# Performance work log

Measured on AMD Instinct MI355X. Metric: run time of the kernel, lower is better.

Reference implementation:

```python
import jax, jax.numpy as jnp
import numpy as np

S, T, SP = 4096, 64, 48          # spatial, temporal, seqPredict
P = T - SP                        # predictLength = 16
INP, EMB_H, EMB = 3, 64, 128      # input size, embedding hidden, embedding size
HID, OUT = 256, 128               # LSTM hidden, outputLayer size
FC1, FC2, LG = 256, 64, 32        # output FCNet dims, laneGate hidden


def setup_inputs() -> dict:
    key = jax.random.key(0)
    ks = jax.random.split(key, 32)
    def w(k, shape, fan_in):
        return jax.random.normal(k, shape, dtype=jnp.float32) / np.sqrt(fan_in)
    inp = {}
    inp["inputData"] = jax.random.normal(ks[0], (S, T, INP), dtype=jnp.float32)
    inp["lane"] = jax.random.uniform(ks[1], (S, 1), dtype=jnp.float32)
    # laneGate FCNet: 1 -> LG -> 1
    inp["lgW1"] = w(ks[2], (LG, 1), 1); inp["lgb1"] = jnp.zeros((LG,), jnp.float32)
    inp["lgW2"] = w(ks[3], (1, LG), LG); inp["lgb2"] = jnp.zeros((1,), jnp.float32)
    # embedding FCNet: INP -> EMB_H -> EMB
    inp["eW1"] = w(ks[4], (EMB_H, INP), INP); inp["eb1"] = jnp.zeros((EMB_H,), jnp.float32)
    inp["eW2"] = w(ks[5], (EMB, EMB_H), EMB_H); inp["eb2"] = jnp.zeros((EMB,), jnp.float32)
    # LSTMCell (gate order i, f, g, o)
    inp["Wih"] = w(ks[6], (4 * HID, EMB), EMB)
    inp["Whh"] = w(ks[7], (4 * HID, HID), HID)
    inp["bih"] = jnp.zeros((4 * HID,), jnp.float32)
    inp["bhh"] = jnp.zeros((4 * HID,), jnp.float32)
    # Conv1d(1,1,3,padding=1)
    inp["convw"] = w(ks[8], (3,), 3)
    inp["convb"] = jnp.zeros((1,), jnp.float32)
    # outputLayer: HID -> OUT
    inp["oW"] = w(ks[9], (OUT, HID), HID); inp["ob"] = jnp.zeros((OUT,), jnp.float32)
    # outputs FCNet (addLayer): OUT -> FC1 -> FC2 -> 1
    inp["fW1"] = w(ks[10], (FC1, OUT), OUT); inp["fb1"] = jnp.zeros((FC1,), jnp.float32)
    inp["fW2"] = w(ks[11], (FC2, FC1), FC1); inp["fb2"] = jnp.zeros((FC2,), jnp.float32)
    inp["fW3"] = w(ks[12], (1, FC2), FC2); inp["fb3"] = jnp.zeros((1,), jnp.float32)
    return inp


def reference(inputData, lane, lgW1, lgb1, lgW2, lgb2, eW1, eb1, eW2, eb2,
              Wih, Whh, bih, bhh, convw, convb, oW, ob,
              fW1, fb1, fW2, fb2, fW3, fb3):
    # laneGate: FCNet(1->LG->1) then sigmoid
    lg = jax.nn.relu(lane @ lgW1.T + lgb1) @ lgW2.T + lgb2
    laneC = jax.nn.sigmoid(lg)                       # [S, 1]
    x = inputData * laneC[:, :, None]                # [S, T, INP]
    # embedding FCNet + outer relu
    emb = jax.nn.relu(jax.nn.relu(x @ eW1.T + eb1) @ eW2.T + eb2)  # [S, T, EMB]
    xs = jnp.transpose(emb, (1, 0, 2))               # [T, S, EMB]

    def convpool(h):
        hp = jnp.pad(h, ((0, 0), (1, 1)))
        return convw[0] * hp[:, :-2] + convw[1] * hp[:, 1:-1] + convw[2] * hp[:, 2:] + convb[0]

    def step(carry, x_t):
        h, c = carry
        g = x_t @ Wih.T + bih + h @ Whh.T + bhh      # [S, 4*HID]
        i, f, gg, o = jnp.split(g, 4, axis=-1)
        c = jax.nn.sigmoid(f) * c + jax.nn.sigmoid(i) * jnp.tanh(gg)
        h = jax.nn.sigmoid(o) * jnp.tanh(c)
        h = convpool(h)
        return (h, c), (h, c)

    h0 = jnp.zeros((S, HID), jnp.float32)
    c0 = jnp.zeros((S, HID), jnp.float32)
    # loop 1: time 0 .. SP inclusive (SP+1 steps)
    (h1, c1), (Hs1, Cs1) = jax.lax.scan(step, (h0, c0), xs[:SP + 1])
    # loop 2: time SP .. T-1 (re-processes step SP, overwriting H[:,:,SP])
    (_, _), (Hs2, Cs2) = jax.lax.scan(step, (h1, c1), xs[SP:])

    H = jnp.transpose(jnp.concatenate([Hs1[:SP], Hs2], axis=0), (1, 2, 0))  # [S, HID, T]
    C = jnp.transpose(jnp.concatenate([Cs1[:SP], Cs2], axis=0), (1, 2, 0))

    predict_h = jnp.transpose(Hs2, (1, 0, 2)).reshape(S * P, HID)
    out = predict_h @ oW.T + ob                      # [S*P, OUT]
    out = jax.nn.relu(out @ fW1.T + fb1)
    out = jax.nn.relu(out @ fW2.T + fb2)
    out = out @ fW3.T + fb3                          # [S*P, 1]
    output = out.reshape(S, P) / laneC               # [S, P]
    return (output, H, C)
```

## Files before the change

### kernel.cpp

```cpp
#include <hip/hip_runtime.h>
#include <hip/hip_bf16.h>
#include <stdint.h>

using f32x4  = __attribute__((ext_vector_type(4))) float;
using bf16x8 = __attribute__((ext_vector_type(8))) __bf16;
using short8 = __attribute__((ext_vector_type(8))) short;

__device__ __forceinline__ short f2b(float f) {
    unsigned u = __builtin_bit_cast(unsigned, f);
    unsigned r = (u + 0x7fff + ((u >> 16) & 1)) >> 16;
    return (short)r;
}
__device__ __forceinline__ float b2f(short s) {
    unsigned u = ((unsigned)(unsigned short)s) << 16;
    return __builtin_bit_cast(float, u);
}
__device__ __forceinline__ float sigf(float x) {
    return __builtin_amdgcn_rcpf(1.f + __expf(-x));
}
__device__ __forceinline__ float tanhf_fast(float x) {
    x = fminf(fmaxf(x, -15.f), 15.f);
    return 2.f * __builtin_amdgcn_rcpf(1.f + __expf(-2.f * x)) - 1.f;
}

__global__ __launch_bounds__(256) void lanec_k(const float* lane, const float* W1, const float* b1,
                                               const float* W2, const float* b2, float* laneC) {
    int s = blockIdx.x * 256 + threadIdx.x;
    float v = lane[s];
    float acc = b2[0];
    #pragma unroll
    for (int k = 0; k < 32; ++k) {
        float t = fmaxf(v * W1[k] + b1[k], 0.f);
        acc += t * W2[k];
    }
    laneC[s] = 1.f / (1.f + __expf(-acc));
}

__global__ __launch_bounds__(256) void pack_k(const float* Wih, const float* Whh, const float* bih,
                                              const float* bhh, const float* oW, const float* fW1,
                                              const float* fW2, const float* eW2,
                                              short* pW2, float* biasP,
                                              short* oWp, short* fW1p, short* fW2p, short* eW2p) {
    int i = blockIdx.x * 256 + threadIdx.x;
    if (i < 393216) {
        int e = i & 7, l = (i >> 3) & 63, fg = (i >> 9) & 63, kc = i >> 15;
        int w = fg >> 3, f = fg & 7;
        int lj = l & 15, lk = l >> 4;
        int g = f >> 1, u = f & 1;
        int j = 32 * w + 16 * u + lj;
        int n = g * 256 + j;
        int k = kc * 32 + lk * 8 + e;
        pW2[i] = f2b(k < 128 ? Wih[n * 128 + k] : Whh[n * 256 + (k - 128)]);
        return;
    }
    i -= 393216;
    if (i < 1024) {
        int lj = i & 15, f = (i >> 4) & 7, w = i >> 7;
        int g = f >> 1, u = f & 1;
        int j = 32 * w + 16 * u + lj;
        int n = g * 256 + j;
        biasP[i] = bih[n] + bhh[n];
        return;
    }
    i -= 1024;
    if (i < 32768) { oWp[i] = f2b(oW[i]); return; }
    i -= 32768;
    if (i < 32768) { fW1p[i] = f2b(fW1[i]); return; }
    i -= 32768;
    if (i < 32768) {
        int n = i / 256;
        fW2p[i] = (n < 64) ? f2b(fW2[i]) : (short)0;
        return;
    }
    i -= 32768;
    if (i < 8192) { eW2p[i] = f2b(eW2[i]); return; }
}

__global__ __launch_bounds__(256) void embed1_k(const float* inp, const float* laneC,
                                                const float* eW1, const float* eb1, short* h1) {
    int g = threadIdx.x >> 6, j = threadIdx.x & 63;
    int t = blockIdx.x >> 10;
    int s = ((blockIdx.x & 1023) << 2) + g;
    float lc = laneC[s];
    size_t rin = ((size_t)s * 64 + t) * 3;
    float x0 = inp[rin] * lc, x1 = inp[rin + 1] * lc, x2 = inp[rin + 2] * lc;
    float h = fmaxf(eW1[j * 3] * x0 + eW1[j * 3 + 1] * x1 + eW1[j * 3 + 2] * x2 + eb1[j], 0.f);
    h1[((size_t)t * 4096 + s) * 64 + j] = f2b(h);
}

__global__ __launch_bounds__(256) void gemm_k(const short* A1, int K1, const short* A2, int K2,
                                              const short* B, int Kt, const float* bias,
                                              float* outF, short* outB, int Nstore, int Nreal,
                                              int relu) {
    __shared__ alignas(16) short As[128 * 32];
    __shared__ alignas(16) short Bs[128 * 32];
    int tid = threadIdx.x;
    int wave = tid >> 6, lane = tid & 63;
    int m0 = blockIdx.x * 128, n0 = blockIdx.y * 128;

    f32x4 acc[4][4];
    #pragma unroll
    for (int i = 0; i < 4; ++i)
        #pragma unroll
        for (int j = 0; j < 4; ++j) acc[i][j] = (f32x4){0.f, 0.f, 0.f, 0.f};

    const int lr = lane & 15, lk8 = (lane >> 4) * 8;
    const int am = (wave & 1) * 64, bn = (wave >> 1) * 64;
    const int row = tid >> 2, c8 = (tid & 3) * 8;
    int nK = Kt / 32;

    for (int kt = 0; kt < nK; ++kt) {
        int kk = kt * 32;
        const short* Asrc; int astr, acol;
        if (kk < K1) { Asrc = A1; astr = K1; acol = kk; }
        else         { Asrc = A2; astr = K2; acol = kk - K1; }
        short8 a0 = *(const short8*)(Asrc + (size_t)(m0 + row) * astr + acol + c8);
        short8 a1 = *(const short8*)(Asrc + (size_t)(m0 + 64 + row) * astr + acol + c8);
        short8 b0 = *(const short8*)(B + (size_t)(n0 + row) * Kt + kk + c8);
        short8 b1 = *(const short8*)(B + (size_t)(n0 + 64 + row) * Kt + kk + c8);
        __syncthreads();
        *(short8*)&As[tid * 8] = a0;
        *(short8*)&As[(tid + 256) * 8] = a1;
        *(short8*)&Bs[tid * 8] = b0;
        *(short8*)&Bs[(tid + 256) * 8] = b1;
        __syncthreads();
        bf16x8 af[4], bfr[4];
        #pragma unroll
        for (int i = 0; i < 4; ++i) af[i]  = *(const bf16x8*)&As[(am + i * 16 + lr) * 32 + lk8];
        #pragma unroll
        for (int j = 0; j < 4; ++j) bfr[j] = *(const bf16x8*)&Bs[(bn + j * 16 + lr) * 32 + lk8];
        #pragma unroll
        for (int i = 0; i < 4; ++i)
            #pragma unroll
            for (int j = 0; j < 4; ++j)
                acc[i][j] = __builtin_amdgcn_mfma_f32_16x16x32_bf16(af[i], bfr[j], acc[i][j], 0, 0, 0);
    }

    int r0 = m0 + am + (lane >> 4) * 4;
    int c0 = n0 + bn + (lane & 15);
    #pragma unroll
    for (int j = 0; j < 4; ++j) {
        int col = c0 + j * 16;
        if (col >= Nreal) continue;
        float bs = bias[col];
        #pragma unroll
        for (int i = 0; i < 4; ++i) {
            #pragma unroll
            for (int r = 0; r < 4; ++r) {
                int rw = r0 + i * 16 + r;
                float v = acc[i][j][r] + bs;
                if (relu) v = fmaxf(v, 0.f);
                size_t o = (size_t)rw * Nstore + col;
                if (outF) outF[o] = v;
                if (outB) outB[o] = f2b(v);
            }
        }
    }
}

__global__ __launch_bounds__(512, 2) void lstm_k(const short* xs, const short* pW2, const float* biasP,
                                                 const float* convw, const float* convb,
                                                 float* Hd, float* Cd, short* predictb, int staged) {
    __shared__ alignas(16) short Wbuf[2][32768];
    __shared__ alignas(16) short h_lds[4096];
    __shared__ float hraw[16][258];

    const int tid = threadIdx.x;
    const int w = tid >> 6, l = tid & 63;
    const int lj = l & 15, lk = l >> 4;
    const int s0 = blockIdx.x * 16;

    bf16x8 wreg[4][8];
    #pragma unroll
    for (int kc = 0; kc < 4; ++kc)
        #pragma unroll
        for (int f = 0; f < 8; ++f)
            wreg[kc][f] = *(const bf16x8*)(pW2 + (size_t)((kc * 64 + w * 8 + f) * 64 + l) * 8);
    float biasv[8];
    #pragma unroll
    for (int f = 0; f < 8; ++f) biasv[f] = biasP[w * 128 + f * 16 + lj];
    float creg[2][4] = {{0.f, 0.f, 0.f, 0.f}, {0.f, 0.f, 0.f, 0.f}};
    const float cw0 = convw[0], cw1 = convw[1], cw2 = convw[2], cb = convb[0];

    for (int i = tid; i < 4096; i += 512) h_lds[i] = 0;
    if (tid < 16) { hraw[tid][0] = 0.f; hraw[tid][257] = 0.f; }
    __syncthreads();

    short* WbufF = &Wbuf[0][0];
    auto issue_chunk = [&](int c, int pp) {
        const short* src = pW2 + (size_t)c * 32768 + tid * 8;
        short* dst = WbufF + pp * 32768 + tid * 8;
        #pragma unroll
        for (int ri = 0; ri < 8; ++ri)
            __builtin_amdgcn_global_load_lds(
                (const __attribute__((address_space(1))) void*)(src + ri * 4096),
                (__attribute__((address_space(3))) void*)(dst + ri * 4096), 16, 0, 0);
    };

    int p = 0;
    issue_chunk(4, 0);

    for (int k = 0; k < 65; ++k) {
        int it = (k <= 48) ? k : k - 1;
        const short* xrow = xs + ((size_t)it * 4096 + s0 + lj) * 128 + lk * 8;
        bf16x8 ax0 = *(const bf16x8*)(xrow);
        bf16x8 ax1 = *(const bf16x8*)(xrow + 32);
        bf16x8 ax2 = *(const bf16x8*)(xrow + 64);
        bf16x8 ax3 = *(const bf16x8*)(xrow + 96);

        f32x4 acc[8];
        #pragma unroll
        for (int f = 0; f < 8; ++f) acc[f] = (f32x4){biasv[f], biasv[f], biasv[f], biasv[f]};
        #pragma unroll
        for (int f = 0; f < 8; ++f) acc[f] = __builtin_amdgcn_mfma_f32_16x16x32_bf16(ax0, wreg[0][f], acc[f], 0, 0, 0);
        #pragma unroll
        for (int f = 0; f < 8; ++f) acc[f] = __builtin_amdgcn_mfma_f32_16x16x32_bf16(ax1, wreg[1][f], acc[f], 0, 0, 0);
        #pragma unroll
        for (int f = 0; f < 8; ++f) acc[f] = __builtin_amdgcn_mfma_f32_16x16x32_bf16(ax2, wreg[2][f], acc[f], 0, 0, 0);
        #pragma unroll
        for (int f = 0; f < 8; ++f) acc[f] = __builtin_amdgcn_mfma_f32_16x16x32_bf16(ax3, wreg[3][f], acc[f], 0, 0, 0);

        #pragma unroll
        for (int cc = 0; cc < 8; ++cc) {
            asm volatile("s_waitcnt vmcnt(0)" ::: "memory");
            __syncthreads();
            issue_chunk(cc < 7 ? cc + 5 : 4, p ^ 1);
            bf16x8 ah = *(const bf16x8*)&h_lds[((cc * 4 + lk) * 16 + lj) * 8];
            #pragma unroll
            for (int f = 0; f < 8; ++f) {
                bf16x8 wf = *(const bf16x8*)(WbufF + p * 32768 + ((w * 8 + f) * 64 + l) * 8);
                acc[f] = __builtin_amdgcn_mfma_f32_16x16x32_bf16(ah, wf, acc[f], 0, 0, 0);
            }
            p ^= 1;
        }

        int tslot = (k < 48) ? k : k - 1;
        int doW = (k != 48);
        int pslot = k - 49;
        #pragma unroll
        for (int u = 0; u < 2; ++u) {
            int j = 32 * w + 16 * u + lj;
            #pragma unroll
            for (int r = 0; r < 4; ++r) {
                int s = 4 * lk + r;
                float gi = acc[0 + u][r], gf = acc[2 + u][r];
                float gg = acc[4 + u][r], go = acc[6 + u][r];
                float c = sigf(gf) * creg[u][r] + sigf(gi) * tanhf_fast(gg);
                creg[u][r] = c;
                hraw[s][j + 1] = sigf(go) * tanhf_fast(c);
                if (doW) {
                    size_t o = staged ? ((((size_t)(s0 + s) * 64 + tslot) << 8) + j)
                                      : ((((size_t)(s0 + s) << 8) + j) * 64 + tslot);
                    Cd[o] = c;
                }
            }
        }
        __syncthreads();

        #pragma unroll
        for (int u = 0; u < 2; ++u) {
            int j = 32 * w + 16 * u + lj;
            int elbase = ((w * 4 + 2 * u + (lj >> 3)) * 16) * 8 + (lj & 7);
            #pragma unroll
            for (int r = 0; r < 4; ++r) {
                int s = 4 * lk + r;
                float h = cw0 * hraw[s][j] + cw1 * hraw[s][j + 1] + cw2 * hraw[s][j + 2] + cb;
                h_lds[elbase + s * 8] = f2b(h);
                if (doW) {
                    size_t o = staged ? ((((size_t)(s0 + s) * 64 + tslot) << 8) + j)
                                      : ((((size_t)(s0 + s) << 8) + j) * 64 + tslot);
                    Hd[o] = h;
                }
                if (pslot >= 0) predictb[(((size_t)(s0 + s) * 16 + pslot) << 8) + j] = f2b(h);
            }
        }
        __syncthreads();
    }
}

__global__ __launch_bounds__(256) void transpose_k(const float* Hs, const float* Cs,
                                                   float* Ho, float* Co) {
    __shared__ float tile[64][129];
    int s = blockIdx.x, jh = blockIdx.y;
    const float* src = blockIdx.z ? Cs : Hs;
    float* dst = blockIdx.z ? Co : Ho;
    #pragma unroll 4
    for (int i = 0; i < 32; ++i) {
        int idx = i * 256 + threadIdx.x;
        int t = idx >> 7, jj = idx & 127;
        tile[t][jj] = src[((size_t)s * 64 + t) * 256 + jh * 128 + jj];
    }
    __syncthreads();
    #pragma unroll 4
    for (int i = 0; i < 32; ++i) {
        int idx = i * 256 + threadIdx.x;
        int jj = idx >> 6, t = idx & 63;
        dst[((size_t)s * 256 + jh * 128 + jj) * 64 + t] = tile[t][jj];
    }
}

__global__ __launch_bounds__(256) void final_k(const short* t2b, const float* fW3, const float* fb3,
                                               const float* laneC, float* out0) {
    int r = blockIdx.x * 256 + threadIdx.x;
    float acc = fb3[0];
    const short* rowp = t2b + (size_t)r * 64;
    #pragma unroll 8
    for (int k = 0; k < 64; ++k) acc += b2f(rowp[k]) * fW3[k];
    out0[r] = acc / laneC[r >> 4];
}

extern "C" void kernel_launch(void* const* d_in, const int* in_sizes, int n_in,
                              void* d_out, int out_size, void* d_ws, size_t ws_size,
                              hipStream_t stream) {
    (void)in_sizes; (void)n_in; (void)out_size;
    const float* inputData = (const float*)d_in[0];
    const float* lane  = (const float*)d_in[1];
    const float* lgW1  = (const float*)d_in[2];  const float* lgb1 = (const float*)d_in[3];
    const float* lgW2  = (const float*)d_in[4];  const float* lgb2 = (const float*)d_in[5];
    const float* eW1   = (const float*)d_in[6];  const float* eb1  = (const float*)d_in[7];
    const float* eW2   = (const float*)d_in[8];  const float* eb2  = (const float*)d_in[9];
    const float* Wih   = (const float*)d_in[10]; const float* Whh  = (const float*)d_in[11];
    const float* bih   = (const float*)d_in[12]; const float* bhh  = (const float*)d_in[13];
    const float* convw = (const float*)d_in[14]; const float* convb= (const float*)d_in[15];
    const float* oW    = (const float*)d_in[16]; const float* ob   = (const float*)d_in[17];
    const float* fW1   = (const float*)d_in[18]; const float* fb1  = (const float*)d_in[19];
    const float* fW2   = (const float*)d_in[20]; const float* fb2  = (const float*)d_in[21];
    const float* fW3   = (const float*)d_in[22]; const float* fb3  = (const float*)d_in[23];

    float* out0 = (float*)d_out;
    float* Hout = out0 + 65536;
    float* Cout = Hout + (size_t)67108864;

    char* w = (char*)d_ws;
    size_t off = 0;
    auto alloc = [&](size_t bytes) -> void* {
        void* p = w + off;
        off += (bytes + 255) & ~(size_t)255;
        return p;
    };
    float* laneC    = (float*)alloc(4096 * 4);
    float* biasP    = (float*)alloc(1024 * 4);
    short* pW2      = (short*)alloc((size_t)1024 * 384 * 2);
    short* oWp      = (short*)alloc((size_t)128 * 256 * 2);
    short* fW1p     = (short*)alloc((size_t)256 * 128 * 2);
    short* fW2p     = (short*)alloc((size_t)128 * 256 * 2);
    short* eW2p     = (short*)alloc((size_t)128 * 64 * 2);
    short* h1       = (short*)alloc((size_t)64 * 4096 * 64 * 2);
    short* xs       = (short*)alloc((size_t)64 * 4096 * 128 * 2);
    short* predictb = (short*)alloc((size_t)65536 * 256 * 2);
    short* t0b      = (short*)alloc((size_t)65536 * 128 * 2);
    short* t1b      = (short*)alloc((size_t)65536 * 256 * 2);
    short* t2b      = (short*)alloc((size_t)65536 * 64 * 2);
    float* Hstage   = (float*)alloc((size_t)4096 * 64 * 256 * 4);
    float* Cstage   = (float*)alloc((size_t)4096 * 64 * 256 * 4);
    bool staged = ws_size >= off;

    lanec_k<<<16, 256, 0, stream>>>(lane, lgW1, lgb1, lgW2, lgb2, laneC);
    {
        int total = 393216 + 1024 + 32768 + 32768 + 32768 + 8192;
        pack_k<<<(total + 255) / 256, 256, 0, stream>>>(Wih, Whh, bih, bhh, oW, fW1, fW2, eW2,
                                                        pW2, biasP, oWp, fW1p, fW2p, eW2p);
    }
    embed1_k<<<65536, 256, 0, stream>>>(inputData, laneC, eW1, eb1, h1);
    gemm_k<<<dim3(2048, 1), 256, 0, stream>>>(h1, 64, (const short*)nullptr, 0, eW2p, 64,
                                              eb2, (float*)nullptr, xs, 128, 128, 1);

    float* Hd = staged ? Hstage : Hout;
    float* Cd = staged ? Cstage : Cout;
    lstm_k<<<256, 512, 0, stream>>>(xs, pW2, biasP, convw, convb, Hd, Cd, predictb,
                                    staged ? 1 : 0);
    if (staged)
        transpose_k<<<dim3(4096, 2, 2), 256, 0, stream>>>(Hstage, Cstage, Hout, Cout);

    gemm_k<<<dim3(512, 1), 256, 0, stream>>>(predictb, 256, (const short*)nullptr, 0, oWp, 256,
                                             ob, (float*)nullptr, t0b, 128, 128, 0);
    gemm_k<<<dim3(512, 2), 256, 0, stream>>>(t0b, 128, (const short*)nullptr, 0, fW1p, 128,
                                             fb1, (float*)nullptr, t1b, 256, 256, 1);
    gemm_k<<<dim3(512, 1), 256, 0, stream>>>(t1b, 256, (const short*)nullptr, 0, fW2p, 256,
                                             fb2, (float*)nullptr, t2b, 64, 64, 1);
    final_k<<<256, 256, 0, stream>>>(t2b, fW3, fb3, laneC, out0);
}
```

Before: 1.833 ms.

## Restructure LSTM kernel: 32 rows per block, streamed weights, shuffle conv, bf16 staging

The LSTM kernel now processes 32 spatial rows per block over 128 blocks instead of 16 rows over 256, so each streamed weight fragment feeds two MFMAs. The input-projection weights are no longer held in registers; all twelve K-chunks (input plus hidden) are double-buffered into LDS per wave. The depthwise conv across the hidden dimension uses lane shuffles plus small edge arrays instead of a full float LDS scratch. H and C are staged in bf16 before the transpose to float, which halves staging traffic but rounds the H/C outputs to bf16 precision. The unstaged fallback path is removed.

```diff
diff --git a/kernel.cpp b/kernel.cpp
--- a/kernel.cpp
+++ b/kernel.cpp
@@ -158,144 +158,176 @@
     }
 }
 
-__global__ __launch_bounds__(512, 2) void lstm_k(const short* xs, const short* pW2, const float* biasP,
+__global__ __launch_bounds__(512, 1) void lstm_k(const short* xs, const short* pW2, const float* biasP,
                                                  const float* convw, const float* convb,
-                                                 float* Hd, float* Cd, short* predictb, int staged) {
-    __shared__ alignas(16) short Wbuf[2][32768];
-    __shared__ alignas(16) short h_lds[4096];
-    __shared__ float hraw[16][258];
+                                                 short* Hd, short* Cd, short* predictb) {
+    __shared__ alignas(16) short Wbuf[2][8][4096];
+    __shared__ alignas(16) short hfrag[8192];
+    __shared__ float edgeA[8][32];
+    __shared__ float edgeB[8][32];
 
     const int tid = threadIdx.x;
     const int w = tid >> 6, l = tid & 63;
     const int lj = l & 15, lk = l >> 4;
-    const int s0 = blockIdx.x * 16;
-
-    bf16x8 wreg[4][8];
-    #pragma unroll
-    for (int kc = 0; kc < 4; ++kc)
-        #pragma unroll
-        for (int f = 0; f < 8; ++f)
-            wreg[kc][f] = *(const bf16x8*)(pW2 + (size_t)((kc * 64 + w * 8 + f) * 64 + l) * 8);
+    const int sb = blockIdx.x * 32;
+
     float biasv[8];
     #pragma unroll
     for (int f = 0; f < 8; ++f) biasv[f] = biasP[w * 128 + f * 16 + lj];
-    float creg[2][4] = {{0.f, 0.f, 0.f, 0.f}, {0.f, 0.f, 0.f, 0.f}};
+    float creg[2][2][4] = {};
     const float cw0 = convw[0], cw1 = convw[1], cw2 = convw[2], cb = convb[0];
 
-    for (int i = tid; i < 4096; i += 512) h_lds[i] = 0;
-    if (tid < 16) { hraw[tid][0] = 0.f; hraw[tid][257] = 0.f; }
+    for (int i = tid; i < 8192; i += 512) hfrag[i] = 0;
     __syncthreads();
 
-    short* WbufF = &Wbuf[0][0];
-    auto issue_chunk = [&](int c, int pp) {
-        const short* src = pW2 + (size_t)c * 32768 + tid * 8;
-        short* dst = WbufF + pp * 32768 + tid * 8;
+    auto issueW = [&](int kc, int pp) {
+        const short* src = pW2 + (((size_t)kc * 64 + w * 8) << 9) + l * 8;
+        short* dst = &Wbuf[pp][w][l * 8];
         #pragma unroll
         for (int ri = 0; ri < 8; ++ri)
             __builtin_amdgcn_global_load_lds(
-                (const __attribute__((address_space(1))) void*)(src + ri * 4096),
-                (__attribute__((address_space(3))) void*)(dst + ri * 4096), 16, 0, 0);
+                (const __attribute__((address_space(1))) void*)(src + ri * 512),
+                (__attribute__((address_space(3))) void*)(dst + ri * 512), 16, 0, 0);
     };
 
-    int p = 0;
-    issue_chunk(4, 0);
+    bf16x8 a[4][2];
+    auto loadA = [&](int it) {
+        #pragma unroll
+        for (int kc = 0; kc < 4; ++kc)
+            #pragma unroll
+            for (int rg = 0; rg < 2; ++rg)
+                a[kc][rg] = *(const bf16x8*)(xs + ((size_t)it * 4096 + sb + rg * 16 + lj) * 128
+                                             + kc * 32 + lk * 8);
+    };
+
+    loadA(0);
+    issueW(0, 0);
+    issueW(1, 1);
 
     for (int k = 0; k < 65; ++k) {
-        int it = (k <= 48) ? k : k - 1;
-        const short* xrow = xs + ((size_t)it * 4096 + s0 + lj) * 128 + lk * 8;
-        bf16x8 ax0 = *(const bf16x8*)(xrow);
-        bf16x8 ax1 = *(const bf16x8*)(xrow + 32);
-        bf16x8 ax2 = *(const bf16x8*)(xrow + 64);
-        bf16x8 ax3 = *(const bf16x8*)(xrow + 96);
-
-        f32x4 acc[8];
-        #pragma unroll
-        for (int f = 0; f < 8; ++f) acc[f] = (f32x4){biasv[f], biasv[f], biasv[f], biasv[f]};
-        #pragma unroll
-        for (int f = 0; f < 8; ++f) acc[f] = __builtin_amdgcn_mfma_f32_16x16x32_bf16(ax0, wreg[0][f], acc[f], 0, 0, 0);
-        #pragma unroll
-        for (int f = 0; f < 8; ++f) acc[f] = __builtin_amdgcn_mfma_f32_16x16x32_bf16(ax1, wreg[1][f], acc[f], 0, 0, 0);
-        #pragma unroll
-        for (int f = 0; f < 8; ++f) acc[f] = __builtin_amdgcn_mfma_f32_16x16x32_bf16(ax2, wreg[2][f], acc[f], 0, 0, 0);
-        #pragma unroll
-        for (int f = 0; f < 8; ++f) acc[f] = __builtin_amdgcn_mfma_f32_16x16x32_bf16(ax3, wreg[3][f], acc[f], 0, 0, 0);
-
-        #pragma unroll
-        for (int cc = 0; cc < 8; ++cc) {
-            asm volatile("s_waitcnt vmcnt(0)" ::: "memory");
-            __syncthreads();
-            issue_chunk(cc < 7 ? cc + 5 : 4, p ^ 1);
-            bf16x8 ah = *(const bf16x8*)&h_lds[((cc * 4 + lk) * 16 + lj) * 8];
+        const int itn = (k < 48) ? k + 1 : ((k < 64) ? k : 63);
+
+        f32x4 acc[2][8];
+        #pragma unroll
+        for (int rg = 0; rg < 2; ++rg)
+            #pragma unroll
+            for (int f = 0; f < 8; ++f)
+                acc[rg][f] = (f32x4){biasv[f], biasv[f], biasv[f], biasv[f]};
+
+        #pragma unroll
+        for (int kc = 0; kc < 12; ++kc) {
+            asm volatile("s_waitcnt vmcnt(8)" ::: "memory");
+            const int p = kc & 1;
+            bf16x8 af0, af1;
+            if (kc < 4) { af0 = a[kc][0]; af1 = a[kc][1]; }
+            else {
+                const int hc = kc - 4;
+                af0 = *(const bf16x8*)&hfrag[(((hc * 4 + lk) * 2 + 0) * 16 + lj) * 8];
+                af1 = *(const bf16x8*)&hfrag[(((hc * 4 + lk) * 2 + 1) * 16 + lj) * 8];
+            }
             #pragma unroll
             for (int f = 0; f < 8; ++f) {
-                bf16x8 wf = *(const bf16x8*)(WbufF + p * 32768 + ((w * 8 + f) * 64 + l) * 8);
-                acc[f] = __builtin_amdgcn_mfma_f32_16x16x32_bf16(ah, wf, acc[f], 0, 0, 0);
+                bf16x8 wf = *(const bf16x8*)&Wbuf[p][w][f * 512 + l * 8];
+                acc[0][f] = __builtin_amdgcn_mfma_f32_16x16x32_bf16(af0, wf, acc[0][f], 0, 0, 0);
+                acc[1][f] = __builtin_amdgcn_mfma_f32_16x16x32_bf16(af1, wf, acc[1][f], 0, 0, 0);
             }
-            p ^= 1;
+            if (kc == 9) loadA(itn);
+            if (kc <= 9) issueW(kc + 2, p);
+            else if (kc == 10) issueW(0, 0);
+            else issueW(1, 1);
         }
 
-        int tslot = (k < 48) ? k : k - 1;
-        int doW = (k != 48);
-        int pslot = k - 49;
-        #pragma unroll
-        for (int u = 0; u < 2; ++u) {
-            int j = 32 * w + 16 * u + lj;
+        float hr[2][2][4];
+        #pragma unroll
+        for (int rg = 0; rg < 2; ++rg)
+            #pragma unroll
+            for (int u = 0; u < 2; ++u)
+                #pragma unroll
+                for (int r = 0; r < 4; ++r) {
+                    float gi = acc[rg][u][r],     gf = acc[rg][2 + u][r];
+                    float gg = acc[rg][4 + u][r], go = acc[rg][6 + u][r];
+                    float c = sigf(gf) * creg[rg][u][r] + sigf(gi) * tanhf_fast(gg);
+                    creg[rg][u][r] = c;
+                    hr[rg][u][r] = sigf(go) * tanhf_fast(c);
+                }
+        if (lj == 0) {
+            #pragma unroll
+            for (int rg = 0; rg < 2; ++rg)
+                #pragma unroll
+                for (int r = 0; r < 4; ++r) edgeA[w][rg * 16 + 4 * lk + r] = hr[rg][0][r];
+        }
+        if (lj == 15) {
+            #pragma unroll
+            for (int rg = 0; rg < 2; ++rg)
+                #pragma unroll
+                for (int r = 0; r < 4; ++r) edgeB[w][rg * 16 + 4 * lk + r] = hr[rg][1][r];
+        }
+        asm volatile("s_waitcnt lgkmcnt(0)" ::: "memory");
+        __builtin_amdgcn_s_barrier();
+
+        const int tslot = (k < 48) ? k : k - 1;
+        const bool doW = (k != 48);
+        const int pslot = k - 49;
+        #pragma unroll
+        for (int rg = 0; rg < 2; ++rg)
             #pragma unroll
             for (int r = 0; r < 4; ++r) {
-                int s = 4 * lk + r;
-                float gi = acc[0 + u][r], gf = acc[2 + u][r];
-                float gg = acc[4 + u][r], go = acc[6 + u][r];
-                float c = sigf(gf) * creg[u][r] + sigf(gi) * tanhf_fast(gg);
-                creg[u][r] = c;
-                hraw[s][j + 1] = sigf(go) * tanhf_fast(c);
+                const int s = rg * 16 + 4 * lk + r;
+                float v0 = hr[rg][0][r], v1 = hr[rg][1][r];
+                float s0r = __shfl(v0, l + 1, 64);
+                float s0l = __shfl(v0, l - 1, 64);
+                float s1r = __shfl(v1, l + 1, 64);
+                float s1l = __shfl(v1, l - 1, 64);
+                float x01 = __shfl(v1, l - 15, 64);
+                float x10 = __shfl(v0, l + 15, 64);
+                float n0r = (lj < 15) ? s0r : x01;
+                float n0l = (lj > 0) ? s0l : (w > 0 ? edgeB[w - 1][s] : 0.f);
+                float n1r = (lj < 15) ? s1r : (w < 7 ? edgeA[w + 1][s] : 0.f);
+                float n1l = (lj > 0) ? s1l : x10;
+                float h0 = cw0 * n0l + cw1 * v0 + cw2 * n0r + cb;
+                float h1 = cw0 * n1l + cw1 * v1 + cw2 * n1r + cb;
+                const int j0 = 32 * w + lj, j1 = j0 + 16;
+                hfrag[(((w * 4 + 0 + (lj >> 3)) * 2 + rg) * 16 + 4 * lk + r) * 8 + (lj & 7)] = f2b(h0);
+                hfrag[(((w * 4 + 2 + (lj >> 3)) * 2 + rg) * 16 + 4 * lk + r) * 8 + (lj & 7)] = f2b(h1);
+                const int ss = sb + s;
                 if (doW) {
-                    size_t o = staged ? ((((size_t)(s0 + s) * 64 + tslot) << 8) + j)
-                                      : ((((size_t)(s0 + s) << 8) + j) * 64 + tslot);
-                    Cd[o] = c;
+                    size_t o0 = ((size_t)ss * 64 + tslot) * 256;
+                    Hd[o0 + j0] = f2b(h0);
+                    Hd[o0 + j1] = f2b(h1);
+                    Cd[o0 + j0] = f2b(creg[rg][0][r]);
+                    Cd[o0 + j1] = f2b(creg[rg][1][r]);
+                }
+                if (pslot >= 0) {
+                    size_t po = ((size_t)ss * 16 + pslot) * 256;
+                    predictb[po + j0] = f2b(h0);
+                    predictb[po + j1] = f2b(h1);
                 }
             }
-        }
-        __syncthreads();
-
-        #pragma unroll
-        for (int u = 0; u < 2; ++u) {
-            int j = 32 * w + 16 * u + lj;
-            int elbase = ((w * 4 + 2 * u + (lj >> 3)) * 16) * 8 + (lj & 7);
-            #pragma unroll
-            for (int r = 0; r < 4; ++r) {
-                int s = 4 * lk + r;
-                float h = cw0 * hraw[s][j] + cw1 * hraw[s][j + 1] + cw2 * hraw[s][j + 2] + cb;
-                h_lds[elbase + s * 8] = f2b(h);
-                if (doW) {
-                    size_t o = staged ? ((((size_t)(s0 + s) * 64 + tslot) << 8) + j)
-                                      : ((((size_t)(s0 + s) << 8) + j) * 64 + tslot);
-                    Hd[o] = h;
-                }
-                if (pslot >= 0) predictb[(((size_t)(s0 + s) * 16 + pslot) << 8) + j] = f2b(h);
-            }
-        }
-        __syncthreads();
-    }
-}
-
-__global__ __launch_bounds__(256) void transpose_k(const float* Hs, const float* Cs,
+        asm volatile("s_waitcnt lgkmcnt(0)" ::: "memory");
+        __builtin_amdgcn_s_barrier();
+    }
+    asm volatile("s_waitcnt vmcnt(0)" ::: "memory");
+}
+
+__global__ __launch_bounds__(256) void transpose_k(const short* Hs, const short* Cs,
                                                    float* Ho, float* Co) {
-    __shared__ float tile[64][129];
+    __shared__ short tile[64][132];
     int s = blockIdx.x, jh = blockIdx.y;
-    const float* src = blockIdx.z ? Cs : Hs;
+    const short* src = blockIdx.z ? Cs : Hs;
     float* dst = blockIdx.z ? Co : Ho;
     #pragma unroll 4
-    for (int i = 0; i < 32; ++i) {
+    for (int i = 0; i < 16; ++i) {
         int idx = i * 256 + threadIdx.x;
-        int t = idx >> 7, jj = idx & 127;
-        tile[t][jj] = src[((size_t)s * 64 + t) * 256 + jh * 128 + jj];
+        int t = idx >> 6, jj2 = idx & 63;
+        *(int*)&tile[t][jj2 * 2] =
+            *(const int*)&src[((size_t)s * 64 + t) * 256 + jh * 128 + jj2 * 2];
     }
     __syncthreads();
     #pragma unroll 4
     for (int i = 0; i < 32; ++i) {
         int idx = i * 256 + threadIdx.x;
         int jj = idx >> 6, t = idx & 63;
-        dst[((size_t)s * 256 + jh * 128 + jj) * 64 + t] = tile[t][jj];
+        dst[((size_t)s * 256 + jh * 128 + jj) * 64 + t] = b2f(tile[t][jj]);
     }
 }
 
@@ -312,7 +344,7 @@
 extern "C" void kernel_launch(void* const* d_in, const int* in_sizes, int n_in,
                               void* d_out, int out_size, void* d_ws, size_t ws_size,
                               hipStream_t stream) {
-    (void)in_sizes; (void)n_in; (void)out_size;
+    (void)in_sizes; (void)n_in; (void)out_size; (void)ws_size;
     const float* inputData = (const float*)d_in[0];
     const float* lane  = (const float*)d_in[1];
     const float* lgW1  = (const float*)d_in[2];  const float* lgb1 = (const float*)d_in[3];
@@ -351,9 +383,8 @@
     short* t0b      = (short*)alloc((size_t)65536 * 128 * 2);
     short* t1b      = (short*)alloc((size_t)65536 * 256 * 2);
     short* t2b      = (short*)alloc((size_t)65536 * 64 * 2);
-    float* Hstage   = (float*)alloc((size_t)4096 * 64 * 256 * 4);
-    float* Cstage   = (float*)alloc((size_t)4096 * 64 * 256 * 4);
-    bool staged = ws_size >= off;
+    short* Hstage   = (short*)alloc((size_t)4096 * 64 * 256 * 2);
+    short* Cstage   = (short*)alloc((size_t)4096 * 64 * 256 * 2);
 
     lanec_k<<<16, 256, 0, stream>>>(lane, lgW1, lgb1, lgW2, lgb2, laneC);
     {
@@ -365,12 +396,9 @@
     gemm_k<<<dim3(2048, 1), 256, 0, stream>>>(h1, 64, (const short*)nullptr, 0, eW2p, 64,
                                               eb2, (float*)nullptr, xs, 128, 128, 1);
 
-    float* Hd = staged ? Hstage : Hout;
-    float* Cd = staged ? Cstage : Cout;
-    lstm_k<<<256, 512, 0, stream>>>(xs, pW2, biasP, convw, convb, Hd, Cd, predictb,
-                                    staged ? 1 : 0);
-    if (staged)
-        transpose_k<<<dim3(4096, 2, 2), 256, 0, stream>>>(Hstage, Cstage, Hout, Cout);
+    lstm_k<<<128, 512, 0, stream>>>(xs, pW2, biasP, convw, convb, Hstage, Cstage, predictb);
+
+    transpose_k<<<dim3(4096, 2, 2), 256, 0, stream>>>(Hstage, Cstage, Hout, Cout);
 
     gemm_k<<<dim3(512, 1), 256, 0, stream>>>(predictb, 256, (const short*)nullptr, 0, oWp, 256,
                                              ob, (float*)nullptr, t0b, 128, 128, 0);
```

Result: slower. 2.814 ms (+53.5%).
